# Optimization experiments

Hardware: AMD Instinct MI355X
Metric: run time of the kernel (lower is better)

## Reference

```python
import jax, jax.numpy as jnp
import numpy as np

B = 1_048_576
NUM_USERS = 6041
NUM_MOVIES = 3953
EMB_DIM = 32
NUM_GENRES = 18
HIDDEN = [64, 32, 16]
WIDE_DIM = NUM_USERS + NUM_MOVIES + 3 + NUM_GENRES  # gender, age, occupation scalars
DEEP_IN = 2 * EMB_DIM + 3 + NUM_GENRES              # = 85


def setup_inputs() -> dict:
    key = jax.random.key(0)
    ks = jax.random.split(key, 20)
    inp = {
        "user_ids": jax.random.randint(ks[0], (B,), 0, NUM_USERS),
        "movie_ids": jax.random.randint(ks[1], (B,), 0, NUM_MOVIES),
        "gender": jax.random.uniform(ks[2], (B,), dtype=jnp.float32),
        "age": jax.random.uniform(ks[3], (B,), dtype=jnp.float32),
        "occupation": jax.random.uniform(ks[4], (B,), dtype=jnp.float32),
        "genres": jax.random.uniform(ks[5], (B, NUM_GENRES), dtype=jnp.float32),
        # wide linear (out_features=1): weight vector + scalar bias
        "wide_W": jax.random.normal(ks[6], (WIDE_DIM,), dtype=jnp.float32) * 0.01,
        "wide_b": jnp.zeros((), dtype=jnp.float32),
        # embedding tables
        "user_table": jax.random.normal(ks[7], (NUM_USERS, EMB_DIM), dtype=jnp.float32) * 0.05,
        "movie_table": jax.random.normal(ks[8], (NUM_MOVIES, EMB_DIM), dtype=jnp.float32) * 0.05,
        # deep MLP params (stored as [in, out])
        "W1": jax.random.normal(ks[9], (DEEP_IN, HIDDEN[0]), dtype=jnp.float32) * 0.05,
        "b1": jnp.zeros((HIDDEN[0],), dtype=jnp.float32),
        "W2": jax.random.normal(ks[10], (HIDDEN[0], HIDDEN[1]), dtype=jnp.float32) * 0.05,
        "b2": jnp.zeros((HIDDEN[1],), dtype=jnp.float32),
        "W3": jax.random.normal(ks[11], (HIDDEN[1], HIDDEN[2]), dtype=jnp.float32) * 0.05,
        "b3": jnp.zeros((HIDDEN[2],), dtype=jnp.float32),
        "W4": jax.random.normal(ks[12], (HIDDEN[2], 1), dtype=jnp.float32) * 0.05,
        "b4": jnp.zeros((1,), dtype=jnp.float32),
    }
    return inp


def reference(user_ids, movie_ids, gender, age, occupation, genres,
              wide_W, wide_b, user_table, movie_table,
              W1, b1, W2, b2, W3, b3, W4, b4):
    nu = user_table.shape[0]
    nm = movie_table.shape[0]
    # dense (non-one-hot) part of the wide input: [B, 3 + num_genres]
    rest = jnp.concatenate(
        [gender[:, None], age[:, None], occupation[:, None], genres], axis=1)
    # one_hot @ W  ==  gather of the corresponding weight entries (same math,
    # without materializing the [B, nu+nm+21] one-hot matrix)
    w_user = wide_W[:nu]
    w_movie = wide_W[nu:nu + nm]
    w_rest = wide_W[nu + nm:]
    wide_out = w_user[user_ids] + w_movie[movie_ids] + rest @ w_rest + wide_b  # [B]

    # deep path (dropout is identity at inference)
    u_emb = user_table[user_ids]    # [B, 32]
    m_emb = movie_table[movie_ids]  # [B, 32]
    h = jnp.concatenate([u_emb, m_emb, rest], axis=1)  # [B, 85]
    h = jax.nn.relu(h @ W1 + b1)
    h = jax.nn.relu(h @ W2 + b2)
    h = jax.nn.relu(h @ W3 + b3)
    deep_out = (h @ W4 + b4)[:, 0]  # [B]

    return jax.nn.sigmoid(wide_out + deep_out)  # [B]
```

## Files before the change

kernel.cpp:

```cpp
#include <hip/hip_runtime.h>

#define NUSERS  6041
#define NMOVIES 3953
#define EMB     32
#define NGEN    18
#define H1N     64
#define H2N     32
#define H3N     16

typedef __bf16 bf16_t;
typedef bf16_t bf16x8 __attribute__((ext_vector_type(8)));
typedef bf16_t bf16x4 __attribute__((ext_vector_type(4)));
typedef float  f32x4  __attribute__((ext_vector_type(4)));
typedef float  f32x8  __attribute__((ext_vector_type(8)));

__device__ __forceinline__ f32x4 mfma16(bf16x8 a, bf16x8 b, f32x4 c) {
    return __builtin_amdgcn_mfma_f32_16x16x32_bf16(a, b, c, 0, 0, 0);
}
__device__ __forceinline__ bf16x8 cvt8(f32x8 v) {
    bf16x8 o;
    #pragma unroll
    for (int i = 0; i < 8; ++i) o[i] = (bf16_t)v[i];
    return o;
}

#define L1STRIDE 68
#define L2STRIDE 36
#define RSTRIDE  28
#define RBUFSZ   (16 * RSTRIDE)

#define RESTW 24

#define TAB_U4   (NUSERS * EMB / 4)
#define TAB_M4   (NMOVIES * EMB / 4)
#define TAB4TOT  (TAB_U4 + TAB_M4)

__global__ __launch_bounds__(256)
void prep_all(const float* __restrict__ gender,
              const float* __restrict__ age,
              const float* __restrict__ occupation,
              const float* __restrict__ genres,
              const float* __restrict__ user_table,
              const float* __restrict__ movie_table,
              bf16_t* __restrict__ rest,
              bf16_t* __restrict__ utab,
              bf16_t* __restrict__ mtab,
              int n)
{
    const int t = blockIdx.x * blockDim.x + threadIdx.x;

    if (t < TAB4TOT) {
        if (t < TAB_U4) {
            float4 v = *(const float4*)(user_table + (size_t)t * 4);
            bf16x4 o; o[0]=(bf16_t)v.x; o[1]=(bf16_t)v.y; o[2]=(bf16_t)v.z; o[3]=(bf16_t)v.w;
            *(bf16x4*)(utab + (size_t)t * 4) = o;
        } else {
            const int u = t - TAB_U4;
            float4 v = *(const float4*)(movie_table + (size_t)u * 4);
            bf16x4 o; o[0]=(bf16_t)v.x; o[1]=(bf16_t)v.y; o[2]=(bf16_t)v.z; o[3]=(bf16_t)v.w;
            *(bf16x4*)(mtab + (size_t)u * 4) = o;
        }
    }

    if (t < n) {
        const float* gr = genres + (size_t)t * NGEN;
        float x[NGEN];
        #pragma unroll
        for (int j = 0; j < 9; ++j) {
            float2 v = *(const float2*)(gr + 2 * j);
            x[2 * j] = v.x; x[2 * j + 1] = v.y;
        }
        const float gg = gender[t], aa = age[t], oo = occupation[t];

        bf16x8 c0, c1, c2;
        c0[0]=(bf16_t)gg;  c0[1]=(bf16_t)aa;  c0[2]=(bf16_t)oo;
        c0[3]=(bf16_t)x[0]; c0[4]=(bf16_t)x[1]; c0[5]=(bf16_t)x[2];
        c0[6]=(bf16_t)x[3]; c0[7]=(bf16_t)x[4];
        #pragma unroll
        for (int j = 0; j < 8; ++j) c1[j] = (bf16_t)x[5 + j];
        #pragma unroll
        for (int j = 0; j < 5; ++j) c2[j] = (bf16_t)x[13 + j];
        c2[5] = (bf16_t)0.0f; c2[6] = (bf16_t)0.0f; c2[7] = (bf16_t)0.0f;

        bf16_t* op = rest + (size_t)t * RESTW;
        *(bf16x8*)(op)      = c0;
        *(bf16x8*)(op + 8)  = c1;
        *(bf16x8*)(op + 16) = c2;
    }
}

__global__ __launch_bounds__(256)
void wd_fwd_main(const int*   __restrict__ user_ids,
                 const int*   __restrict__ movie_ids,
                 const float* __restrict__ wide_W,
                 const float* __restrict__ wide_b,
                 const float* __restrict__ W1,
                 const float* __restrict__ b1,
                 const float* __restrict__ W2,
                 const float* __restrict__ b2,
                 const float* __restrict__ W3,
                 const float* __restrict__ b3,
                 const float* __restrict__ W4,
                 const float* __restrict__ b4,
                 const bf16_t* __restrict__ utab,
                 const bf16_t* __restrict__ mtab,
                 const bf16_t* __restrict__ rest,
                 float*       __restrict__ out,
                 int n)
{
    const int lane = threadIdx.x & 63;
    const int wib  = threadIdx.x >> 6;
    const int m    = lane & 15;
    const int quad = lane >> 4;

    __shared__ float lds1[4][16 * L1STRIDE];
    __shared__ float lds2[4][16 * L2STRIDE];
    float* __restrict__ L1p = lds1[wib];
    float* __restrict__ L2p = lds2[wib];

    bf16x8 B1f[3][4];
    #pragma unroll
    for (int kt = 0; kt < 3; ++kt)
        #pragma unroll
        for (int nt = 0; nt < 4; ++nt) {
            bf16x8 f;
            #pragma unroll
            for (int j = 0; j < 8; ++j) {
                const int k  = kt * 32 + quad * 8 + j;
                const float v = (k < 85) ? W1[k * H1N + nt * 16 + m] : 0.0f;
                f[j] = (bf16_t)v;
            }
            B1f[kt][nt] = f;
        }
    bf16x8 Bwf;
    {
        const float* wr = wide_W + NUSERS + NMOVIES;
        #pragma unroll
        for (int j = 0; j < 8; ++j) {
            const int k = 64 + quad * 8 + j;
            float v = 0.0f;
            if (m == 0) { if (k < 85) v = wr[k - 64]; else if (k == 85) v = 1.0f; }
            Bwf[j] = (bf16_t)v;
        }
    }
    bf16x8 B2f[2][2];
    #pragma unroll
    for (int kt = 0; kt < 2; ++kt)
        #pragma unroll
        for (int nt = 0; nt < 2; ++nt) {
            bf16x8 f;
            #pragma unroll
            for (int j = 0; j < 8; ++j)
                f[j] = (bf16_t)W2[(kt * 32 + quad * 8 + j) * H2N + nt * 16 + m];
            B2f[kt][nt] = f;
        }
    bf16x8 B3f;
    #pragma unroll
    for (int j = 0; j < 8; ++j) B3f[j] = (bf16_t)W3[(quad * 8 + j) * H3N + m];

    float bias1[4], bias2[2];
    #pragma unroll
    for (int nt = 0; nt < 4; ++nt) bias1[nt] = b1[nt * 16 + m];
    #pragma unroll
    for (int nt = 0; nt < 2; ++nt) bias2[nt] = b2[nt * 16 + m];
    const float bias3 = b3[m];
    const float w4v   = W4[m];
    const float b4v   = b4[0];
    const float wb0   = wide_b[0];

    const int ntiles = (n + 15) >> 4;
    const int gwave  = blockIdx.x * 4 + wib;
    const int nwaves = gridDim.x * 4;
    int niter = 0;
    if (gwave < ntiles) niter = (ntiles - gwave + nwaves - 1) / nwaves;
    if (niter == 0) return;

    int t_c = gwave;
    int t_n = t_c + nwaves; if (t_n >= ntiles) t_n = t_c;

    int rc = t_c * 16 + m; if (rc >= n) rc = n - 1;
    int uid_c = user_ids[rc], mid_c = movie_ids[rc];
    bf16x8 A2c;
    #pragma unroll
    for (int j = 0; j < 8; ++j) A2c[j] = (bf16_t)0.0f;
    if (quad < 3) A2c = *(const bf16x8*)(rest + (size_t)rc * RESTW + quad * 8);
    float wuc = 0.0f, wmc = 0.0f;
    if (quad == 2) { wuc = wide_W[uid_c]; wmc = wide_W[NUSERS + mid_c]; }

    for (int i = 0; i < niter; ++i) {
        const bf16x8 A0 = *(const bf16x8*)(utab + (size_t)uid_c * EMB + quad * 8);
        const bf16x8 A1 = *(const bf16x8*)(mtab + (size_t)mid_c * EMB + quad * 8);

        const bool more = (i + 1 < niter);
        int uid_n = uid_c, mid_n = mid_c;
        bf16x8 A2n = A2c;
        float wun = wuc, wmn = wmc;
        int t_n2 = t_n;
        if (more) {
            int rn = t_n * 16 + m; if (rn >= n) rn = n - 1;
            uid_n = user_ids[rn]; mid_n = movie_ids[rn];
            #pragma unroll
            for (int j = 0; j < 8; ++j) A2n[j] = (bf16_t)0.0f;
            if (quad < 3) A2n = *(const bf16x8*)(rest + (size_t)rn * RESTW + quad * 8);
            wun = 0.0f; wmn = 0.0f;
            if (quad == 2) { wun = wide_W[uid_n]; wmn = wide_W[NUSERS + mid_n]; }
            t_n2 = t_n + nwaves; if (t_n2 >= ntiles) t_n2 = t_n;
        }

        const int base = t_c << 4;
        bf16x8 A2 = A2c;
        if (quad == 2) A2[5] = (bf16_t)(wuc + wmc + wb0);

        f32x4 accw = mfma16(A2, Bwf, (f32x4){0.f, 0.f, 0.f, 0.f});

        f32x4 acc[4];
        #pragma unroll
        for (int nt = 0; nt < 4; ++nt) {
            f32x4 c = {bias1[nt], bias1[nt], bias1[nt], bias1[nt]};
            c = mfma16(A2, B1f[2][nt], c);
            c = mfma16(A1, B1f[1][nt], c);
            c = mfma16(A0, B1f[0][nt], c);
            acc[nt] = c;
        }
        #pragma unroll
        for (int nt = 0; nt < 4; ++nt)
            #pragma unroll
            for (int r = 0; r < 4; ++r)
                L1p[(quad * 4 + r) * L1STRIDE + nt * 16 + m] = fmaxf(acc[nt][r], 0.0f);

        bf16x8 AL2[2];
        #pragma unroll
        for (int kt = 0; kt < 2; ++kt) {
            const float4* s = (const float4*)(L1p + m * L1STRIDE + kt * 32 + quad * 8);
            float4 a = s[0], b = s[1];
            f32x8 t8; t8[0]=a.x; t8[1]=a.y; t8[2]=a.z; t8[3]=a.w;
            t8[4]=b.x; t8[5]=b.y; t8[6]=b.z; t8[7]=b.w;
            AL2[kt] = cvt8(t8);
        }

        f32x4 acc2[2];
        #pragma unroll
        for (int nt = 0; nt < 2; ++nt) {
            f32x4 c = {bias2[nt], bias2[nt], bias2[nt], bias2[nt]};
            c = mfma16(AL2[0], B2f[0][nt], c);
            c = mfma16(AL2[1], B2f[1][nt], c);
            acc2[nt] = c;
        }
        #pragma unroll
        for (int nt = 0; nt < 2; ++nt)
            #pragma unroll
            for (int r = 0; r < 4; ++r)
                L2p[(quad * 4 + r) * L2STRIDE + nt * 16 + m] = fmaxf(acc2[nt][r], 0.0f);

        bf16x8 AL3;
        {
            const float4* s = (const float4*)(L2p + m * L2STRIDE + quad * 8);
            float4 a = s[0], b = s[1];
            f32x8 t8; t8[0]=a.x; t8[1]=a.y; t8[2]=a.z; t8[3]=a.w;
            t8[4]=b.x; t8[5]=b.y; t8[6]=b.z; t8[7]=b.w;
            AL3 = cvt8(t8);
        }

        f32x4 acc3 = mfma16(AL3, B3f, (f32x4){bias3, bias3, bias3, bias3});

        float t0 = fmaxf(acc3[0], 0.0f) * w4v + accw[0];
        float t1 = fmaxf(acc3[1], 0.0f) * w4v + accw[1];
        float t2 = fmaxf(acc3[2], 0.0f) * w4v + accw[2];
        float t3 = fmaxf(acc3[3], 0.0f) * w4v + accw[3];
        #pragma unroll
        for (int off = 1; off < 16; off <<= 1) {
            t0 += __shfl_xor(t0, off, 64);
            t1 += __shfl_xor(t1, off, 64);
            t2 += __shfl_xor(t2, off, 64);
            t3 += __shfl_xor(t3, off, 64);
        }
        if (m < 4) {
            float zv = t0;
            zv = (m == 1) ? t1 : zv;
            zv = (m == 2) ? t2 : zv;
            zv = (m == 3) ? t3 : zv;
            zv += b4v;
            const int orow = base + quad * 4 + m;
            if (orow < n) out[orow] = 1.0f / (1.0f + __expf(-zv));
        }

        if (more) {
            A2c = A2n; wuc = wun; wmc = wmn;
            uid_c = uid_n; mid_c = mid_n;
            t_c = t_n; t_n = t_n2;
        }
    }
}

struct Pref {
    float4 u0, u1, m0, m1;
    float  wu, wm;
};

__global__ __launch_bounds__(256)
void wd_fwd_pipe(const int*   __restrict__ user_ids,
                 const int*   __restrict__ movie_ids,
                 const float* __restrict__ gender,
                 const float* __restrict__ age,
                 const float* __restrict__ occupation,
                 const float* __restrict__ genres,
                 const float* __restrict__ wide_W,
                 const float* __restrict__ wide_b,
                 const float* __restrict__ user_table,
                 const float* __restrict__ movie_table,
                 const float* __restrict__ W1,
                 const float* __restrict__ b1,
                 const float* __restrict__ W2,
                 const float* __restrict__ b2,
                 const float* __restrict__ W3,
                 const float* __restrict__ b3,
                 const float* __restrict__ W4,
                 const float* __restrict__ b4,
                 float*       __restrict__ out,
                 int n)
{
    const int lane = threadIdx.x & 63;
    const int wib  = threadIdx.x >> 6;
    const int m    = lane & 15;
    const int quad = lane >> 4;

    __shared__ float lds_rest[4][2 * RBUFSZ];
    __shared__ float lds1[4][16 * L1STRIDE];
    __shared__ float lds2[4][16 * L2STRIDE];
    float* __restrict__ rbase = lds_rest[wib];
    float* __restrict__ L1p   = lds1[wib];
    float* __restrict__ L2p   = lds2[wib];

    for (int k = lane; k < 2 * RBUFSZ; k += 64) rbase[k] = 0.0f;

    bf16x8 B1f[3][4];
    #pragma unroll
    for (int kt = 0; kt < 3; ++kt)
        #pragma unroll
        for (int nt = 0; nt < 4; ++nt) {
            bf16x8 f;
            #pragma unroll
            for (int j = 0; j < 8; ++j) {
                const int k  = kt * 32 + quad * 8 + j;
                const float v = (k < 85) ? W1[k * H1N + nt * 16 + m] : 0.0f;
                f[j] = (bf16_t)v;
            }
            B1f[kt][nt] = f;
        }
    bf16x8 Bwf;
    {
        const float* wr = wide_W + NUSERS + NMOVIES;
        #pragma unroll
        for (int j = 0; j < 8; ++j) {
            const int k = 64 + quad * 8 + j;
            float v = 0.0f;
            if (m == 0) { if (k < 85) v = wr[k - 64]; else if (k == 85) v = 1.0f; }
            Bwf[j] = (bf16_t)v;
        }
    }
    bf16x8 B2f[2][2];
    #pragma unroll
    for (int kt = 0; kt < 2; ++kt)
        #pragma unroll
        for (int nt = 0; nt < 2; ++nt) {
            bf16x8 f;
            #pragma unroll
            for (int j = 0; j < 8; ++j)
                f[j] = (bf16_t)W2[(kt * 32 + quad * 8 + j) * H2N + nt * 16 + m];
            B2f[kt][nt] = f;
        }
    bf16x8 B3f;
    #pragma unroll
    for (int j = 0; j < 8; ++j) B3f[j] = (bf16_t)W3[(quad * 8 + j) * H3N + m];

    float bias1[4], bias2[2];
    #pragma unroll
    for (int nt = 0; nt < 4; ++nt) bias1[nt] = b1[nt * 16 + m];
    #pragma unroll
    for (int nt = 0; nt < 2; ++nt) bias2[nt] = b2[nt * 16 + m];
    const float bias3 = b3[m];
    const float w4v   = W4[m];
    const float b4v   = b4[0];
    const float wb0   = wide_b[0];

    const int ntiles = (n + 15) >> 4;
    const int gwave  = blockIdx.x * 4 + wib;
    const int nwaves = gridDim.x * 4;
    int niter = 0;
    if (gwave < ntiles) niter = (ntiles - gwave + nwaves - 1) / nwaves;
    const long gmax = (long)n * NGEN - 1;

#define LOAD_IDS(tt, U, M) { int rr = (tt) * 16 + m; rr = rr < n ? rr : n - 1; \
                             U = user_ids[rr]; M = movie_ids[rr]; }
#define LOAD_GENRES(tt, G, SC) { \
    const long gb = (long)(tt) * (16 * NGEN); \
    _Pragma("unroll") \
    for (int r = 0; r < 4; ++r) { long idx = gb + lane + r * 64; \
        idx = idx < gmax ? idx : gmax; G[r] = genres[idx]; } \
    { long idx = gb + lane + 256; idx = idx < gmax ? idx : gmax; \
      G[4] = (lane < 32) ? genres[idx] : 0.0f; } \
    { int rr = (tt) * 16 + m; rr = rr < n ? rr : n - 1; \
      const float* sp = (quad == 0) ? gender : (quad == 1) ? age : occupation; \
      SC = (quad < 3) ? sp[rr] : 0.0f; } }
#define WRITE_RBUF(B, G, SC) { \
    float* rb_ = rbase + (B) * RBUFSZ; \
    _Pragma("unroll") \
    for (int r = 0; r < 4; ++r) { int gi = lane + r * 64; int rw = gi / NGEN; \
        int cl = gi - rw * NGEN; rb_[rw * RSTRIDE + 3 + cl] = G[r]; } \
    if (lane < 32) { int gi = lane + 256; int rw = gi / NGEN; int cl = gi - rw * NGEN; \
        rb_[rw * RSTRIDE + 3 + cl] = G[4]; } \
    if (quad < 3) rb_[m * RSTRIDE + quad] = SC; }
#define ISSUE_GATHER(UID, MID, P) { \
    const float4* up_ = (const float4*)(user_table + (size_t)(UID) * EMB + quad * 8); \
    P.u0 = up_[0]; P.u1 = up_[1]; \
    const float4* mp_ = (const float4*)(movie_table + (size_t)(MID) * EMB + quad * 8); \
    P.m0 = mp_[0]; P.m1 = mp_[1]; \
    P.wu = wide_W[UID]; P.wm = wide_W[NUSERS + (MID)]; }

    if (niter > 0) {
        int t_c = gwave;
        int t_n = t_c + nwaves; if (t_n >= ntiles) t_n = t_c;

        int uid_c, mid_c, uid_n, mid_n, uid_n2, mid_n2;
        float gg_c[5], sc_c, gg_n[5], sc_n;
        Pref P_c, P_n;

        LOAD_IDS(t_c, uid_c, mid_c);
        LOAD_GENRES(t_c, gg_c, sc_c);
        ISSUE_GATHER(uid_c, mid_c, P_c);
        LOAD_IDS(t_n, uid_n, mid_n);
        WRITE_RBUF(0, gg_c, sc_c);
        uid_n2 = uid_n; mid_n2 = mid_n;
        int buf = 0;

        for (int i = 0; i < niter; ++i) {
            const float* rb = rbase + buf * RBUFSZ;
            const float4* sA = (const float4*)(rb + m * RSTRIDE + quad * 8);
            float4 a2a = sA[0], a2b = sA[1];

            const bool more = (i + 1 < niter);
            int t_n2 = t_n;
            if (more) {
                LOAD_GENRES(t_n, gg_n, sc_n);
                ISSUE_GATHER(uid_n, mid_n, P_n);
                t_n2 = t_n + nwaves; if (t_n2 >= ntiles) t_n2 = t_n;
                LOAD_IDS(t_n2, uid_n2, mid_n2);
            }

            const int base = t_c << 4;
            f32x8 vf;
            vf[0]=P_c.u0.x; vf[1]=P_c.u0.y; vf[2]=P_c.u0.z; vf[3]=P_c.u0.w;
            vf[4]=P_c.u1.x; vf[5]=P_c.u1.y; vf[6]=P_c.u1.z; vf[7]=P_c.u1.w;
            bf16x8 A0 = cvt8(vf);
            vf[0]=P_c.m0.x; vf[1]=P_c.m0.y; vf[2]=P_c.m0.z; vf[3]=P_c.m0.w;
            vf[4]=P_c.m1.x; vf[5]=P_c.m1.y; vf[6]=P_c.m1.z; vf[7]=P_c.m1.w;
            bf16x8 A1 = cvt8(vf);
            vf[0]=a2a.x; vf[1]=a2a.y; vf[2]=a2a.z; vf[3]=a2a.w;
            vf[4]=a2b.x; vf[5]=a2b.y; vf[6]=a2b.z; vf[7]=a2b.w;
            if (quad == 2) vf[5] = P_c.wu + P_c.wm + wb0;
            bf16x8 A2 = cvt8(vf);

            f32x4 accw = mfma16(A2, Bwf, (f32x4){0.f, 0.f, 0.f, 0.f});

            f32x4 acc[4];
            #pragma unroll
            for (int nt = 0; nt < 4; ++nt) {
                f32x4 c = {bias1[nt], bias1[nt], bias1[nt], bias1[nt]};
                c = mfma16(A0, B1f[0][nt], c);
                c = mfma16(A1, B1f[1][nt], c);
                c = mfma16(A2, B1f[2][nt], c);
                acc[nt] = c;
            }
            #pragma unroll
            for (int nt = 0; nt < 4; ++nt)
                #pragma unroll
                for (int r = 0; r < 4; ++r)
                    L1p[(quad * 4 + r) * L1STRIDE + nt * 16 + m] = fmaxf(acc[nt][r], 0.0f);

            bf16x8 AL2[2];
            #pragma unroll
            for (int kt = 0; kt < 2; ++kt) {
                const float4* s = (const float4*)(L1p + m * L1STRIDE + kt * 32 + quad * 8);
                float4 a = s[0], b = s[1];
                f32x8 t8; t8[0]=a.x; t8[1]=a.y; t8[2]=a.z; t8[3]=a.w;
                t8[4]=b.x; t8[5]=b.y; t8[6]=b.z; t8[7]=b.w;
                AL2[kt] = cvt8(t8);
            }

            f32x4 acc2[2];
            #pragma unroll
            for (int nt = 0; nt < 2; ++nt) {
                f32x4 c = {bias2[nt], bias2[nt], bias2[nt], bias2[nt]};
                c = mfma16(AL2[0], B2f[0][nt], c);
                c = mfma16(AL2[1], B2f[1][nt], c);
                acc2[nt] = c;
            }
            #pragma unroll
            for (int nt = 0; nt < 2; ++nt)
                #pragma unroll
                for (int r = 0; r < 4; ++r)
                    L2p[(quad * 4 + r) * L2STRIDE + nt * 16 + m] = fmaxf(acc2[nt][r], 0.0f);

            bf16x8 AL3;
            {
                const float4* s = (const float4*)(L2p + m * L2STRIDE + quad * 8);
                float4 a = s[0], b = s[1];
                f32x8 t8; t8[0]=a.x; t8[1]=a.y; t8[2]=a.z; t8[3]=a.w;
                t8[4]=b.x; t8[5]=b.y; t8[6]=b.z; t8[7]=b.w;
                AL3 = cvt8(t8);
            }

            f32x4 acc3 = mfma16(AL3, B3f, (f32x4){bias3, bias3, bias3, bias3});

            float t0 = fmaxf(acc3[0], 0.0f) * w4v + accw[0];
            float t1 = fmaxf(acc3[1], 0.0f) * w4v + accw[1];
            float t2 = fmaxf(acc3[2], 0.0f) * w4v + accw[2];
            float t3 = fmaxf(acc3[3], 0.0f) * w4v + accw[3];
            #pragma unroll
            for (int off = 1; off < 16; off <<= 1) {
                t0 += __shfl_xor(t0, off, 64);
                t1 += __shfl_xor(t1, off, 64);
                t2 += __shfl_xor(t2, off, 64);
                t3 += __shfl_xor(t3, off, 64);
            }
            if (m < 4) {
                float zv = t0;
                zv = (m == 1) ? t1 : zv;
                zv = (m == 2) ? t2 : zv;
                zv = (m == 3) ? t3 : zv;
                zv += b4v;
                const int orow = base + quad * 4 + m;
                if (orow < n) out[orow] = 1.0f / (1.0f + __expf(-zv));
            }

            if (more) {
                WRITE_RBUF(buf ^ 1, gg_n, sc_n);
                P_c = P_n;
                uid_c = uid_n; mid_c = mid_n;
                uid_n = uid_n2; mid_n = mid_n2;
                t_c = t_n; t_n = t_n2;
                buf ^= 1;
            }
        }
    }
#undef LOAD_IDS
#undef LOAD_GENRES
#undef WRITE_RBUF
#undef ISSUE_GATHER
}

extern "C" void kernel_launch(void* const* d_in, const int* in_sizes, int n_in,
                              void* d_out, int out_size, void* d_ws, size_t ws_size,
                              hipStream_t stream)
{
    const int*   user_ids   = (const int*)  d_in[0];
    const int*   movie_ids  = (const int*)  d_in[1];
    const float* gender     = (const float*)d_in[2];
    const float* age        = (const float*)d_in[3];
    const float* occupation = (const float*)d_in[4];
    const float* genres     = (const float*)d_in[5];
    const float* wide_W     = (const float*)d_in[6];
    const float* wide_b     = (const float*)d_in[7];
    const float* user_table = (const float*)d_in[8];
    const float* movie_table= (const float*)d_in[9];
    const float* W1         = (const float*)d_in[10];
    const float* b1         = (const float*)d_in[11];
    const float* W2         = (const float*)d_in[12];
    const float* b2         = (const float*)d_in[13];
    const float* W3         = (const float*)d_in[14];
    const float* b3         = (const float*)d_in[15];
    const float* W4         = (const float*)d_in[16];
    const float* b4         = (const float*)d_in[17];
    float*       out        = (float*)d_out;

    const int n = in_sizes[0];

    const size_t utab_bytes = ((size_t)NUSERS  * EMB * 2 + 255) & ~(size_t)255;
    const size_t mtab_bytes = ((size_t)NMOVIES * EMB * 2 + 255) & ~(size_t)255;
    const size_t rest_bytes = (size_t)n * RESTW * 2;
    const size_t need = utab_bytes + mtab_bytes + rest_bytes;

    if (d_ws != nullptr && ws_size >= need) {
        bf16_t* utab = (bf16_t*)d_ws;
        bf16_t* mtab = (bf16_t*)((char*)d_ws + utab_bytes);
        bf16_t* rest = (bf16_t*)((char*)d_ws + utab_bytes + mtab_bytes);

        const int prep_threads = (n > TAB4TOT) ? n : TAB4TOT;
        const int prep_blocks  = (prep_threads + 255) / 256;
        prep_all<<<prep_blocks, 256, 0, stream>>>(gender, age, occupation, genres,
                                                  user_table, movie_table,
                                                  rest, utab, mtab, n);
        wd_fwd_main<<<1024, 256, 0, stream>>>(user_ids, movie_ids, wide_W, wide_b,
                                              W1, b1, W2, b2, W3, b3, W4, b4,
                                              utab, mtab, rest, out, n);
    } else {
        wd_fwd_pipe<<<1024, 256, 0, stream>>>(user_ids, movie_ids, gender, age, occupation,
                                              genres, wide_W, wide_b, user_table, movie_table,
                                              W1, b1, W2, b2, W3, b3, W4, b4, out, n);
    }
}
```

Measured before the change: 241.3 us.

## Keep MLP activations in registers via transposed MFMA and stage genres through LDS

The main kernel swaps the MFMA operand order so each layer's output lands directly in the register layout the next layer needs. This removes the per-layer LDS round trips and the final 16-lane shuffle reduction. Bias 1 is folded into the matmul through a constant 1.0 column in the packed rest rows, and embedding gathers are prefetched one tile further ahead. The prep kernel now loads genres with coalesced float4 reads into shared memory and splits table conversion into separate blocks, at the cost of more register pressure and permuted weight layouts that must be kept consistent.

```diff
diff --git a/kernel.cpp b/kernel.cpp
--- a/kernel.cpp
+++ b/kernel.cpp
@@ -30,10 +30,31 @@
 #define RBUFSZ   (16 * RSTRIDE)
 
 #define RESTW 24
+#define PREPROWS 512
 
 #define TAB_U4   (NUSERS * EMB / 4)
 #define TAB_M4   (NMOVIES * EMB / 4)
 #define TAB4TOT  (TAB_U4 + TAB_M4)
+
+__device__ __forceinline__ void pack_rest_row(const float* __restrict__ x,
+                                              float gg, float aa, float oo,
+                                              bf16_t* __restrict__ op)
+{
+    bf16x8 c0, c1, c2;
+    c0[0] = (bf16_t)gg;   c0[1] = (bf16_t)aa;   c0[2] = (bf16_t)oo;
+    c0[3] = (bf16_t)x[0]; c0[4] = (bf16_t)x[1]; c0[5] = (bf16_t)x[2];
+    c0[6] = (bf16_t)x[3]; c0[7] = (bf16_t)x[4];
+    #pragma unroll
+    for (int j = 0; j < 8; ++j) c1[j] = (bf16_t)x[5 + j];
+    #pragma unroll
+    for (int j = 0; j < 5; ++j) c2[j] = (bf16_t)x[13 + j];
+    c2[5] = (bf16_t)0.0f;
+    c2[6] = (bf16_t)1.0f;
+    c2[7] = (bf16_t)0.0f;
+    *(bf16x8*)(op)      = c0;
+    *(bf16x8*)(op + 8)  = c1;
+    *(bf16x8*)(op + 16) = c2;
+}
 
 __global__ __launch_bounds__(256)
 void prep_all(const float* __restrict__ gender,
@@ -47,49 +68,68 @@
               bf16_t* __restrict__ mtab,
               int n)
 {
-    const int t = blockIdx.x * blockDim.x + threadIdx.x;
-
-    if (t < TAB4TOT) {
-        if (t < TAB_U4) {
-            float4 v = *(const float4*)(user_table + (size_t)t * 4);
-            bf16x4 o; o[0]=(bf16_t)v.x; o[1]=(bf16_t)v.y; o[2]=(bf16_t)v.z; o[3]=(bf16_t)v.w;
-            *(bf16x4*)(utab + (size_t)t * 4) = o;
+    const int t  = threadIdx.x;
+    const int b  = blockIdx.x;
+    const int gB = (n + PREPROWS - 1) / PREPROWS;
+
+    if (b < gB) {
+        const int r0 = b * PREPROWS;
+        if ((n & 1) == 0) {
+            __shared__ float gbuf[PREPROWS * NGEN];
+            const float4* gsrc = (const float4*)genres;
+            const int totF4  = (n * NGEN) >> 2;
+            const int f4base = (r0 >> 1) * 9;
+            #pragma unroll
+            for (int s = 0; s < 9; ++s) {
+                const int gi = t + s * 256;
+                int idx = f4base + gi;
+                if (idx > totF4 - 1) idx = totF4 - 1;
+                *(float4*)(gbuf + gi * 4) = gsrc[idx];
+            }
+            __syncthreads();
+            #pragma unroll
+            for (int rr = 0; rr < 2; ++rr) {
+                const int lr = t + rr * 256;
+                const int r  = r0 + lr;
+                if (r < n) {
+                    float x[NGEN];
+                    #pragma unroll
+                    for (int c = 0; c < NGEN; ++c) x[c] = gbuf[lr * NGEN + c];
+                    pack_rest_row(x, gender[r], age[r], occupation[r],
+                                  rest + (size_t)r * RESTW);
+                }
+            }
         } else {
-            const int u = t - TAB_U4;
-            float4 v = *(const float4*)(movie_table + (size_t)u * 4);
-            bf16x4 o; o[0]=(bf16_t)v.x; o[1]=(bf16_t)v.y; o[2]=(bf16_t)v.z; o[3]=(bf16_t)v.w;
-            *(bf16x4*)(mtab + (size_t)u * 4) = o;
-        }
-    }
-
-    if (t < n) {
-        const float* gr = genres + (size_t)t * NGEN;
-        float x[NGEN];
-        #pragma unroll
-        for (int j = 0; j < 9; ++j) {
-            float2 v = *(const float2*)(gr + 2 * j);
-            x[2 * j] = v.x; x[2 * j + 1] = v.y;
-        }
-        const float gg = gender[t], aa = age[t], oo = occupation[t];
-
-        bf16x8 c0, c1, c2;
-        c0[0]=(bf16_t)gg;  c0[1]=(bf16_t)aa;  c0[2]=(bf16_t)oo;
-        c0[3]=(bf16_t)x[0]; c0[4]=(bf16_t)x[1]; c0[5]=(bf16_t)x[2];
-        c0[6]=(bf16_t)x[3]; c0[7]=(bf16_t)x[4];
-        #pragma unroll
-        for (int j = 0; j < 8; ++j) c1[j] = (bf16_t)x[5 + j];
-        #pragma unroll
-        for (int j = 0; j < 5; ++j) c2[j] = (bf16_t)x[13 + j];
-        c2[5] = (bf16_t)0.0f; c2[6] = (bf16_t)0.0f; c2[7] = (bf16_t)0.0f;
-
-        bf16_t* op = rest + (size_t)t * RESTW;
-        *(bf16x8*)(op)      = c0;
-        *(bf16x8*)(op + 8)  = c1;
-        *(bf16x8*)(op + 16) = c2;
+            for (int rr = 0; rr < 2; ++rr) {
+                const int r = r0 + t + rr * 256;
+                if (r < n) {
+                    const float* gr = genres + (size_t)r * NGEN;
+                    float x[NGEN];
+                    #pragma unroll
+                    for (int c = 0; c < NGEN; ++c) x[c] = gr[c];
+                    pack_rest_row(x, gender[r], age[r], occupation[r],
+                                  rest + (size_t)r * RESTW);
+                }
+            }
+        }
+    } else {
+        const int u = (b - gB) * 256 + t;
+        if (u < TAB4TOT) {
+            if (u < TAB_U4) {
+                float4 v = *(const float4*)(user_table + (size_t)u * 4);
+                bf16x4 o; o[0]=(bf16_t)v.x; o[1]=(bf16_t)v.y; o[2]=(bf16_t)v.z; o[3]=(bf16_t)v.w;
+                *(bf16x4*)(utab + (size_t)u * 4) = o;
+            } else {
+                const int w = u - TAB_U4;
+                float4 v = *(const float4*)(movie_table + (size_t)w * 4);
+                bf16x4 o; o[0]=(bf16_t)v.x; o[1]=(bf16_t)v.y; o[2]=(bf16_t)v.z; o[3]=(bf16_t)v.w;
+                *(bf16x4*)(mtab + (size_t)w * 4) = o;
+            }
+        }
     }
 }
 
-__global__ __launch_bounds__(256)
+__global__ __launch_bounds__(256, 4)
 void wd_fwd_main(const int*   __restrict__ user_ids,
                  const int*   __restrict__ movie_ids,
                  const float* __restrict__ wide_W,
@@ -109,15 +149,9 @@
                  int n)
 {
     const int lane = threadIdx.x & 63;
-    const int wib  = threadIdx.x >> 6;
     const int m    = lane & 15;
     const int quad = lane >> 4;
 
-    __shared__ float lds1[4][16 * L1STRIDE];
-    __shared__ float lds2[4][16 * L2STRIDE];
-    float* __restrict__ L1p = lds1[wib];
-    float* __restrict__ L2p = lds2[wib];
-
     bf16x8 B1f[3][4];
     #pragma unroll
     for (int kt = 0; kt < 3; ++kt)
@@ -126,8 +160,11 @@
             bf16x8 f;
             #pragma unroll
             for (int j = 0; j < 8; ++j) {
-                const int k  = kt * 32 + quad * 8 + j;
-                const float v = (k < 85) ? W1[k * H1N + nt * 16 + m] : 0.0f;
+                const int k = kt * 32 + quad * 8 + j;
+                float v;
+                if (k < 85)       v = W1[k * H1N + nt * 16 + m];
+                else if (k == 86) v = b1[nt * 16 + m];
+                else              v = 0.0f;
                 f[j] = (bf16_t)v;
             }
             B1f[kt][nt] = f;
@@ -150,27 +187,30 @@
         for (int nt = 0; nt < 2; ++nt) {
             bf16x8 f;
             #pragma unroll
-            for (int j = 0; j < 8; ++j)
-                f[j] = (bf16_t)W2[(kt * 32 + quad * 8 + j) * H2N + nt * 16 + m];
+            for (int j = 0; j < 8; ++j) {
+                const int u = (2 * kt + (j >> 2)) * 16 + quad * 4 + (j & 3);
+                f[j] = (bf16_t)W2[u * H2N + nt * 16 + m];
+            }
             B2f[kt][nt] = f;
         }
     bf16x8 B3f;
     #pragma unroll
-    for (int j = 0; j < 8; ++j) B3f[j] = (bf16_t)W3[(quad * 8 + j) * H3N + m];
-
-    float bias1[4], bias2[2];
-    #pragma unroll
-    for (int nt = 0; nt < 4; ++nt) bias1[nt] = b1[nt * 16 + m];
-    #pragma unroll
-    for (int nt = 0; nt < 2; ++nt) bias2[nt] = b2[nt * 16 + m];
-    const float bias3 = b3[m];
-    const float w4v   = W4[m];
-    const float b4v   = b4[0];
-    const float wb0   = wide_b[0];
+    for (int j = 0; j < 8; ++j) {
+        const int u = (j >> 2) * 16 + quad * 4 + (j & 3);
+        B3f[j] = (bf16_t)W3[u * H3N + m];
+    }
+
+    f32x4 bias2[2], bias3, w4f;
+    bias2[0] = *(const f32x4*)(b2 + quad * 4);
+    bias2[1] = *(const f32x4*)(b2 + 16 + quad * 4);
+    bias3    = *(const f32x4*)(b3 + quad * 4);
+    w4f      = *(const f32x4*)(W4 + quad * 4);
+    const float b4v = b4[0];
+    const float wb0 = wide_b[0];
 
     const int ntiles = (n + 15) >> 4;
-    const int gwave  = blockIdx.x * 4 + wib;
-    const int nwaves = gridDim.x * 4;
+    const int gwave  = (blockIdx.x * blockDim.x + threadIdx.x) >> 6;
+    const int nwaves = (gridDim.x * blockDim.x) >> 6;
     int niter = 0;
     if (gwave < ntiles) niter = (ntiles - gwave + nwaves - 1) / nwaves;
     if (niter == 0) return;
@@ -180,113 +220,100 @@
 
     int rc = t_c * 16 + m; if (rc >= n) rc = n - 1;
     int uid_c = user_ids[rc], mid_c = movie_ids[rc];
+    bf16x8 A0c = *(const bf16x8*)(utab + (size_t)uid_c * EMB + quad * 8);
+    bf16x8 A1c = *(const bf16x8*)(mtab + (size_t)mid_c * EMB + quad * 8);
     bf16x8 A2c;
     #pragma unroll
     for (int j = 0; j < 8; ++j) A2c[j] = (bf16_t)0.0f;
     if (quad < 3) A2c = *(const bf16x8*)(rest + (size_t)rc * RESTW + quad * 8);
     float wuc = 0.0f, wmc = 0.0f;
     if (quad == 2) { wuc = wide_W[uid_c]; wmc = wide_W[NUSERS + mid_c]; }
+    int rn = t_n * 16 + m; if (rn >= n) rn = n - 1;
+    int uid_n = user_ids[rn], mid_n = movie_ids[rn];
 
     for (int i = 0; i < niter; ++i) {
-        const bf16x8 A0 = *(const bf16x8*)(utab + (size_t)uid_c * EMB + quad * 8);
-        const bf16x8 A1 = *(const bf16x8*)(mtab + (size_t)mid_c * EMB + quad * 8);
-
         const bool more = (i + 1 < niter);
-        int uid_n = uid_c, mid_n = mid_c;
-        bf16x8 A2n = A2c;
+        bf16x8 A0n = A0c, A1n = A1c, A2n;
+        #pragma unroll
+        for (int j = 0; j < 8; ++j) A2n[j] = (bf16_t)0.0f;
         float wun = wuc, wmn = wmc;
+        int uid_n2 = uid_n, mid_n2 = mid_n;
         int t_n2 = t_n;
         if (more) {
-            int rn = t_n * 16 + m; if (rn >= n) rn = n - 1;
-            uid_n = user_ids[rn]; mid_n = movie_ids[rn];
-            #pragma unroll
-            for (int j = 0; j < 8; ++j) A2n[j] = (bf16_t)0.0f;
-            if (quad < 3) A2n = *(const bf16x8*)(rest + (size_t)rn * RESTW + quad * 8);
+            A0n = *(const bf16x8*)(utab + (size_t)uid_n * EMB + quad * 8);
+            A1n = *(const bf16x8*)(mtab + (size_t)mid_n * EMB + quad * 8);
+            int rx = t_n * 16 + m; if (rx >= n) rx = n - 1;
+            if (quad < 3) A2n = *(const bf16x8*)(rest + (size_t)rx * RESTW + quad * 8);
             wun = 0.0f; wmn = 0.0f;
             if (quad == 2) { wun = wide_W[uid_n]; wmn = wide_W[NUSERS + mid_n]; }
             t_n2 = t_n + nwaves; if (t_n2 >= ntiles) t_n2 = t_n;
-        }
-
-        const int base = t_c << 4;
+            int r2 = t_n2 * 16 + m; if (r2 >= n) r2 = n - 1;
+            uid_n2 = user_ids[r2]; mid_n2 = movie_ids[r2];
+        }
+
         bf16x8 A2 = A2c;
         if (quad == 2) A2[5] = (bf16_t)(wuc + wmc + wb0);
 
-        f32x4 accw = mfma16(A2, Bwf, (f32x4){0.f, 0.f, 0.f, 0.f});
+        f32x4 accw = mfma16(Bwf, A2, (f32x4){0.f, 0.f, 0.f, 0.f});
 
         f32x4 acc[4];
         #pragma unroll
         for (int nt = 0; nt < 4; ++nt) {
-            f32x4 c = {bias1[nt], bias1[nt], bias1[nt], bias1[nt]};
-            c = mfma16(A2, B1f[2][nt], c);
-            c = mfma16(A1, B1f[1][nt], c);
-            c = mfma16(A0, B1f[0][nt], c);
+            f32x4 c = {0.f, 0.f, 0.f, 0.f};
+            c = mfma16(B1f[2][nt], A2,  c);
+            c = mfma16(B1f[1][nt], A1c, c);
+            c = mfma16(B1f[0][nt], A0c, c);
             acc[nt] = c;
         }
-        #pragma unroll
-        for (int nt = 0; nt < 4; ++nt)
-            #pragma unroll
-            for (int r = 0; r < 4; ++r)
-                L1p[(quad * 4 + r) * L1STRIDE + nt * 16 + m] = fmaxf(acc[nt][r], 0.0f);
 
         bf16x8 AL2[2];
         #pragma unroll
         for (int kt = 0; kt < 2; ++kt) {
-            const float4* s = (const float4*)(L1p + m * L1STRIDE + kt * 32 + quad * 8);
-            float4 a = s[0], b = s[1];
-            f32x8 t8; t8[0]=a.x; t8[1]=a.y; t8[2]=a.z; t8[3]=a.w;
-            t8[4]=b.x; t8[5]=b.y; t8[6]=b.z; t8[7]=b.w;
-            AL2[kt] = cvt8(t8);
+            bf16x8 f;
+            #pragma unroll
+            for (int r = 0; r < 4; ++r) {
+                f[r]     = (bf16_t)fmaxf(acc[2 * kt][r],     0.0f);
+                f[4 + r] = (bf16_t)fmaxf(acc[2 * kt + 1][r], 0.0f);
+            }
+            AL2[kt] = f;
         }
 
         f32x4 acc2[2];
         #pragma unroll
         for (int nt = 0; nt < 2; ++nt) {
-            f32x4 c = {bias2[nt], bias2[nt], bias2[nt], bias2[nt]};
-            c = mfma16(AL2[0], B2f[0][nt], c);
-            c = mfma16(AL2[1], B2f[1][nt], c);
+            f32x4 c = bias2[nt];
+            c = mfma16(B2f[0][nt], AL2[0], c);
+            c = mfma16(B2f[1][nt], AL2[1], c);
             acc2[nt] = c;
         }
-        #pragma unroll
-        for (int nt = 0; nt < 2; ++nt)
-            #pragma unroll
-            for (int r = 0; r < 4; ++r)
-                L2p[(quad * 4 + r) * L2STRIDE + nt * 16 + m] = fmaxf(acc2[nt][r], 0.0f);
 
         bf16x8 AL3;
-        {
-            const float4* s = (const float4*)(L2p + m * L2STRIDE + quad * 8);
-            float4 a = s[0], b = s[1];
-            f32x8 t8; t8[0]=a.x; t8[1]=a.y; t8[2]=a.z; t8[3]=a.w;
-            t8[4]=b.x; t8[5]=b.y; t8[6]=b.z; t8[7]=b.w;
-            AL3 = cvt8(t8);
-        }
-
-        f32x4 acc3 = mfma16(AL3, B3f, (f32x4){bias3, bias3, bias3, bias3});
-
-        float t0 = fmaxf(acc3[0], 0.0f) * w4v + accw[0];
-        float t1 = fmaxf(acc3[1], 0.0f) * w4v + accw[1];
-        float t2 = fmaxf(acc3[2], 0.0f) * w4v + accw[2];
-        float t3 = fmaxf(acc3[3], 0.0f) * w4v + accw[3];
-        #pragma unroll
-        for (int off = 1; off < 16; off <<= 1) {
-            t0 += __shfl_xor(t0, off, 64);
-            t1 += __shfl_xor(t1, off, 64);
-            t2 += __shfl_xor(t2, off, 64);
-            t3 += __shfl_xor(t3, off, 64);
-        }
-        if (m < 4) {
-            float zv = t0;
-            zv = (m == 1) ? t1 : zv;
-            zv = (m == 2) ? t2 : zv;
-            zv = (m == 3) ? t3 : zv;
-            zv += b4v;
-            const int orow = base + quad * 4 + m;
-            if (orow < n) out[orow] = 1.0f / (1.0f + __expf(-zv));
+        #pragma unroll
+        for (int r = 0; r < 4; ++r) {
+            AL3[r]     = (bf16_t)fmaxf(acc2[0][r], 0.0f);
+            AL3[4 + r] = (bf16_t)fmaxf(acc2[1][r], 0.0f);
+        }
+
+        f32x4 acc3 = mfma16(B3f, AL3, bias3);
+
+        float p = fmaxf(acc3[0], 0.0f) * w4f[0]
+                + fmaxf(acc3[1], 0.0f) * w4f[1]
+                + fmaxf(acc3[2], 0.0f) * w4f[2]
+                + fmaxf(acc3[3], 0.0f) * w4f[3];
+        p += __shfl_xor(p, 16, 64);
+        p += __shfl_xor(p, 32, 64);
+        if (lane < 16) {
+            const int orow = (t_c << 4) + lane;
+            if (orow < n) {
+                const float zv = p + accw[0] + b4v;
+                out[orow] = 1.0f / (1.0f + __expf(-zv));
+            }
         }
 
         if (more) {
-            A2c = A2n; wuc = wun; wmc = wmn;
-            uid_c = uid_n; mid_c = mid_n;
+            A0c = A0n; A1c = A1n; A2c = A2n;
+            wuc = wun; wmc = wmn;
+            uid_n = uid_n2; mid_n = mid_n2;
             t_c = t_n; t_n = t_n2;
         }
     }
@@ -585,11 +612,11 @@
         bf16_t* mtab = (bf16_t*)((char*)d_ws + utab_bytes);
         bf16_t* rest = (bf16_t*)((char*)d_ws + utab_bytes + mtab_bytes);
 
-        const int prep_threads = (n > TAB4TOT) ? n : TAB4TOT;
-        const int prep_blocks  = (prep_threads + 255) / 256;
-        prep_all<<<prep_blocks, 256, 0, stream>>>(gender, age, occupation, genres,
-                                                  user_table, movie_table,
-                                                  rest, utab, mtab, n);
+        const int gB      = (n + PREPROWS - 1) / PREPROWS;
+        const int tblocks = (TAB4TOT + 255) / 256;
+        prep_all<<<gB + tblocks, 256, 0, stream>>>(gender, age, occupation, genres,
+                                                   user_table, movie_table,
+                                                   rest, utab, mtab, n);
         wd_fwd_main<<<1024, 256, 0, stream>>>(user_ids, movie_ids, wide_W, wide_b,
                                               W1, b1, W2, b2, W3, b3, W4, b4,
                                               utab, mtab, rest, out, n);
```

Result: slower. 308.7 us (+27.9%).
